# Performance work log

Measured on AMD Instinct MI355X. Metric: run time of the kernel, lower is better.

## Reference

```python
import jax, jax.numpy as jnp
import numpy as np

B = 2
C = 256
NH = 8
DH = C // NH
NL = 4
NP = 4
NLAYERS = 6
DFF = 1024
SHAPES = [(128, 128), (64, 64), (32, 32), (16, 16)]
LQ = sum(h * w for h, w in SHAPES)
STARTS = np.cumsum([0] + [h * w for h, w in SHAPES])[:-1].tolist()


def _ln(x, g, b, eps=1e-5):
    mu = jnp.mean(x, -1, keepdims=True)
    var = jnp.mean((x - mu) ** 2, -1, keepdims=True)
    return (x - mu) * jax.lax.rsqrt(var + eps) * g + b


def _ref_points():
    # centers of each cell, normalized to [0,1]; valid_ratios == 1 (masks=None path)
    pts = []
    for (h, w) in SHAPES:
        ry = (np.arange(h) + 0.5) / h
        rx = (np.arange(w) + 0.5) / w
        gy, gx = np.meshgrid(ry, rx, indexing='ij')
        pts.append(np.stack([gx.reshape(-1), gy.reshape(-1)], -1))
    return jnp.asarray(np.concatenate(pts, 0), jnp.float32)  # [LQ,2] (x,y)


def _bilinear(vf, loc, Hl, Wl):
    # vf: [B,NH,S,DH] flattened level features; loc: [B,LQ,NH,NP,2] in [0,1]
    # grid_sample semantics: bilinear, zero padding, align_corners=False
    x = loc[..., 0] * Wl - 0.5
    y = loc[..., 1] * Hl - 0.5
    x0 = jnp.floor(x)
    y0 = jnp.floor(y)
    wx = x - x0
    wy = y - y0
    out = 0.0
    for dx, dy, w in ((0, 0, (1 - wx) * (1 - wy)), (1, 0, wx * (1 - wy)),
                      (0, 1, (1 - wx) * wy), (1, 1, wx * wy)):
        xi = x0 + dx
        yi = y0 + dy
        valid = (xi >= 0) & (xi < Wl) & (yi >= 0) & (yi < Hl)
        idx = (jnp.clip(yi, 0, Hl - 1) * Wl + jnp.clip(xi, 0, Wl - 1)).astype(jnp.int32)
        idx = jnp.transpose(idx, (0, 2, 1, 3)).reshape(B, NH, -1)  # [B,NH,LQ*NP]
        g = jnp.take_along_axis(vf, idx[..., None], axis=2)        # [B,NH,LQ*NP,DH]
        wgt = jnp.transpose(w * valid, (0, 2, 1, 3)).reshape(B, NH, -1)
        out = out + g * wgt[..., None]
    return out.reshape(B, NH, LQ, NP, DH)


def _forward(src0, src1, src2, src3, pos0, pos1, pos2, pos3, level_embed,
             Woff, boff, Wattn, battn, Wval, bval, Wout, bout,
             g1, b1, Wff1, bff1, Wff2, bff2, g2, b2):
    srcs = [src0, src1, src2, src3]
    poss = [pos0, pos1, pos2, pos3]
    src = jnp.concatenate([s.reshape(B, C, -1).transpose(0, 2, 1) for s in srcs], 1)
    pos = jnp.concatenate([p.reshape(B, C, -1).transpose(0, 2, 1) + level_embed[l][None, None]
                           for l, p in enumerate(poss)], 1)
    ref = _ref_points()  # [LQ,2]
    norm_wh = jnp.asarray([[w, h] for (h, w) in SHAPES], jnp.float32)  # offset_normalizer
    x = src
    for l in range(NLAYERS):
        q = x + pos
        off = (q @ Woff[l] + boff[l]).reshape(B, LQ, NH, NL, NP, 2)
        attn = jax.nn.softmax((q @ Wattn[l] + battn[l]).reshape(B, LQ, NH, NL * NP), -1)
        attn = attn.reshape(B, LQ, NH, NL, NP)
        val = (x @ Wval[l] + bval[l]).reshape(B, LQ, NH, DH)
        loc = ref[None, :, None, None, None, :] + off / norm_wh[None, None, None, :, None, :]
        out = jnp.zeros((B, NH, LQ, DH), x.dtype)
        for lv, (h, w) in enumerate(SHAPES):
            s0 = STARTS[lv]
            vf = val[:, s0:s0 + h * w].transpose(0, 2, 1, 3)   # [B,NH,S,DH]
            samp = _bilinear(vf, loc[:, :, :, lv], h, w)       # [B,NH,LQ,NP,DH]
            a = attn[:, :, :, lv].transpose(0, 2, 1, 3)        # [B,NH,LQ,NP]
            out = out + jnp.einsum('bhqpd,bhqp->bhqd', samp, a)
        out = out.transpose(0, 2, 1, 3).reshape(B, LQ, C) @ Wout[l] + bout[l]
        x = _ln(x + out, g1[l], b1[l])
        ff = jax.nn.relu(x @ Wff1[l] + bff1[l]) @ Wff2[l] + bff2[l]
        x = _ln(x + ff, g2[l], b2[l])
    return x


def setup_inputs() -> dict:
    key = jax.random.key(0)
    ks = jax.random.split(key, 20)
    d = {}
    for i, (h, w) in enumerate(SHAPES):
        d[f'src{i}'] = jax.random.normal(ks[i], (B, C, h, w), jnp.float32)
        d[f'pos{i}'] = jax.random.normal(ks[4 + i], (B, C, h, w), jnp.float32) * 0.1
    d['level_embed'] = jax.random.normal(ks[8], (NL, C), jnp.float32)

    def lin(k, fi, fo, scale=None):
        s = scale if scale is not None else 1.0 / np.sqrt(fi)
        return jax.random.normal(k, (NLAYERS, fi, fo), jnp.float32) * s

    d['Woff'] = lin(ks[9], C, NH * NL * NP * 2, 0.01)
    d['boff'] = jax.random.uniform(ks[10], (NLAYERS, NH * NL * NP * 2), jnp.float32, -0.5, 0.5)
    d['Wattn'] = lin(ks[11], C, NH * NL * NP)
    d['battn'] = jnp.zeros((NLAYERS, NH * NL * NP), jnp.float32)
    d['Wval'] = lin(ks[12], C, C)
    d['bval'] = jnp.zeros((NLAYERS, C), jnp.float32)
    d['Wout'] = lin(ks[13], C, C)
    d['bout'] = jnp.zeros((NLAYERS, C), jnp.float32)
    d['g1'] = jnp.ones((NLAYERS, C), jnp.float32)
    d['b1'] = jnp.zeros((NLAYERS, C), jnp.float32)
    d['Wff1'] = lin(ks[14], C, DFF)
    d['bff1'] = jnp.zeros((NLAYERS, DFF), jnp.float32)
    d['Wff2'] = lin(ks[15], DFF, C)
    d['bff2'] = jnp.zeros((NLAYERS, C), jnp.float32)
    d['g2'] = jnp.ones((NLAYERS, C), jnp.float32)
    d['b2'] = jnp.zeros((NLAYERS, C), jnp.float32)
    return d


def reference(src0, src1, src2, src3, pos0, pos1, pos2, pos3, level_embed,
              Woff, boff, Wattn, battn, Wval, bval, Wout, bout,
              g1, b1, Wff1, bff1, Wff2, bff2, g2, b2):
    return _forward(src0, src1, src2, src3, pos0, pos1, pos2, pos3, level_embed,
                    Woff, boff, Wattn, battn, Wval, bval, Wout, bout,
                    g1, b1, Wff1, bff1, Wff2, bff2, g2, b2)
```

## Files before the change

kernel.cpp:

```cpp
#include <hip/hip_runtime.h>
#include <hip/hip_bf16.h>
#include <math.h>

namespace {
constexpr int B_   = 2;
constexpr int C_   = 256;
constexpr int NH_  = 8;
constexpr int DH_  = 32;
constexpr int NP_  = 4;
constexpr int DFF_ = 1024;
constexpr int LQ_  = 21760;
constexpr int M_   = B_ * LQ_;
}

typedef __bf16  bf16x8 __attribute__((ext_vector_type(8)));
typedef short   s16x8  __attribute__((ext_vector_type(8)));
typedef float   f32x4  __attribute__((ext_vector_type(4)));

static __device__ __forceinline__ unsigned short f2bf(float f) {
    return __builtin_bit_cast(unsigned short, __float2bfloat16(f));
}
static __device__ __forceinline__ float bf2f(unsigned short u) {
    return __bfloat162float(__builtin_bit_cast(__hip_bfloat16, u));
}

__global__ void k_wt(const float* __restrict__ in, __hip_bfloat16* __restrict__ out,
                     int K, int N, int outStride)
{
    __shared__ float tile[32][33];
    int n0 = blockIdx.x * 32, k0 = blockIdx.y * 32;
    const float* inl = in + (size_t)blockIdx.z * K * N;
    __hip_bfloat16* outl = out + (size_t)blockIdx.z * outStride;
    for (int i = threadIdx.y; i < 32; i += 8)
        tile[i][threadIdx.x] = inl[(size_t)(k0 + i) * N + n0 + threadIdx.x];
    __syncthreads();
    for (int i = threadIdx.y; i < 32; i += 8)
        outl[(size_t)(n0 + i) * K + k0 + threadIdx.x] = __float2bfloat16(tile[threadIdx.x][i]);
}

__global__ __launch_bounds__(256) void k_assemble2(
    const float* __restrict__ s0, const float* __restrict__ s1,
    const float* __restrict__ s2, const float* __restrict__ s3,
    const float* __restrict__ p0, const float* __restrict__ p1,
    const float* __restrict__ p2, const float* __restrict__ p3,
    const float* __restrict__ lev, float* __restrict__ x,
    __hip_bfloat16* __restrict__ xbf, __hip_bfloat16* __restrict__ posbf,
    __hip_bfloat16* __restrict__ qbf)
{
    int bid = blockIdx.x;
    int lv, rem, HW, S0;
    const float *sp, *pp;
    if (bid < 8192)       { lv = 0; rem = bid;         HW = 16384; S0 = 0;     sp = s0; pp = p0; }
    else if (bid < 10240) { lv = 1; rem = bid - 8192;  HW = 4096;  S0 = 16384; sp = s1; pp = p1; }
    else if (bid < 10752) { lv = 2; rem = bid - 10240; HW = 1024;  S0 = 20480; sp = s2; pp = p2; }
    else                  { lv = 3; rem = bid - 10752; HW = 256;   S0 = 21504; sp = s3; pp = p3; }
    int sptiles = HW >> 5;
    int spt = rem % sptiles;
    int ct  = (rem / sptiles) & 7;
    int b   = rem / (sptiles * 8);
    int sp0 = spt * 32, c0 = ct * 32;

    __shared__ float ts[32][33], tp[32][33];
    int tx = threadIdx.x & 31, ty = threadIdx.x >> 5;
#pragma unroll
    for (int i = 0; i < 4; i++) {
        int c = c0 + ty + i * 8;
        size_t si = ((size_t)(b * C_ + c)) * HW + sp0 + tx;
        ts[ty + i * 8][tx] = sp[si];
        tp[ty + i * 8][tx] = pp[si];
    }
    __syncthreads();
#pragma unroll
    for (int i = 0; i < 4; i++) {
        int s = S0 + sp0 + ty + i * 8;
        int c = c0 + tx;
        float sv = ts[tx][ty + i * 8];
        float pv = tp[tx][ty + i * 8] + lev[lv * C_ + c];
        size_t idx = ((size_t)(b * LQ_ + s)) * C_ + c;
        x[idx]     = sv;
        xbf[idx]   = __float2bfloat16(sv);
        posbf[idx] = __float2bfloat16(pv);
        qbf[idx]   = __float2bfloat16(sv + pv);
    }
}

template<bool RELU, bool BF16OUT>
__global__ __launch_bounds__(256) void k_gemm_mfma(
    const __hip_bfloat16* __restrict__ A,
    const __hip_bfloat16* __restrict__ Wt,
    const float* __restrict__ bias,
    void* __restrict__ Co,
    int M, int N, int K)
{
    __shared__ char As[128 * 128];
    __shared__ char Bs[128 * 128];
    int t = threadIdx.x, w = t >> 6, lane = t & 63;
    int m0 = blockIdx.x * 128, n0 = blockIdx.y * 128;
    int wm = w >> 1, wn = w & 1;

    f32x4 acc[4][4] = {};

    int rowoff  = lane >> 3;
    int colswz  = ((lane & 7) ^ (lane >> 3)) << 3;

    for (int kt = 0; kt < K; kt += 64) {
#pragma unroll
        for (int j = 0; j < 4; j++) {
            int rowbase = w * 32 + j * 8;
            const __hip_bfloat16* srcA = A  + (size_t)(m0 + rowbase + rowoff) * K + kt + colswz;
            const __hip_bfloat16* srcB = Wt + (size_t)(n0 + rowbase + rowoff) * K + kt + colswz;
            __builtin_amdgcn_global_load_lds(
                (const __attribute__((address_space(1))) void*)srcA,
                (__attribute__((address_space(3))) void*)(As + rowbase * 128), 16, 0, 0);
            __builtin_amdgcn_global_load_lds(
                (const __attribute__((address_space(1))) void*)srcB,
                (__attribute__((address_space(3))) void*)(Bs + rowbase * 128), 16, 0, 0);
        }
        __syncthreads();
#pragma unroll
        for (int k0 = 0; k0 < 64; k0 += 32) {
            int kb = k0 * 2 + (lane >> 4) * 16;
            bf16x8 af[4], bfr[4];
#pragma unroll
            for (int mi = 0; mi < 4; mi++) {
                int r = wm * 64 + mi * 16 + (lane & 15);
                s16x8 raw = *(const s16x8*)(As + r * 128 + (kb ^ ((r & 7) << 4)));
                af[mi] = __builtin_bit_cast(bf16x8, raw);
            }
#pragma unroll
            for (int ni = 0; ni < 4; ni++) {
                int r = wn * 64 + ni * 16 + (lane & 15);
                s16x8 raw = *(const s16x8*)(Bs + r * 128 + (kb ^ ((r & 7) << 4)));
                bfr[ni] = __builtin_bit_cast(bf16x8, raw);
            }
#pragma unroll
            for (int mi = 0; mi < 4; mi++)
#pragma unroll
                for (int ni = 0; ni < 4; ni++)
                    acc[mi][ni] = __builtin_amdgcn_mfma_f32_16x16x32_bf16(
                        af[mi], bfr[ni], acc[mi][ni], 0, 0, 0);
        }
        __syncthreads();
    }

#pragma unroll
    for (int ni = 0; ni < 4; ni++) {
        int col = n0 + wn * 64 + ni * 16 + (lane & 15);
        float bb = bias[col];
#pragma unroll
        for (int mi = 0; mi < 4; mi++) {
            int row = m0 + wm * 64 + mi * 16 + ((lane >> 4) << 2);
#pragma unroll
            for (int r = 0; r < 4; r++) {
                float v = acc[mi][ni][r] + bb;
                if (RELU) v = fmaxf(v, 0.f);
                if (BF16OUT)
                    ((__hip_bfloat16*)Co)[(size_t)(row + r) * N + col] = __float2bfloat16(v);
                else
                    ((float*)Co)[(size_t)(row + r) * N + col] = v;
            }
        }
    }
}

__global__ __launch_bounds__(256) void k_gemm_qa(
    const __hip_bfloat16* __restrict__ A,
    const __hip_bfloat16* __restrict__ Wq,
    const float* __restrict__ boff, const float* __restrict__ battn,
    float* __restrict__ offb, float* __restrict__ attb, int M)
{
    constexpr int K = 256;
    __shared__ char As[128 * 128];
    __shared__ char Bs[128 * 128];
    int t = threadIdx.x, w = t >> 6, lane = t & 63;
    int m0 = blockIdx.x * 128, n0 = blockIdx.y * 128;
    int wm = w >> 1, wn = w & 1;

    f32x4 acc[4][4] = {};
    int rowoff  = lane >> 3;
    int colswz  = ((lane & 7) ^ (lane >> 3)) << 3;

    for (int kt = 0; kt < K; kt += 64) {
#pragma unroll
        for (int j = 0; j < 4; j++) {
            int rowbase = w * 32 + j * 8;
            const __hip_bfloat16* srcA = A  + (size_t)(m0 + rowbase + rowoff) * K + kt + colswz;
            const __hip_bfloat16* srcB = Wq + (size_t)(n0 + rowbase + rowoff) * K + kt + colswz;
            __builtin_amdgcn_global_load_lds(
                (const __attribute__((address_space(1))) void*)srcA,
                (__attribute__((address_space(3))) void*)(As + rowbase * 128), 16, 0, 0);
            __builtin_amdgcn_global_load_lds(
                (const __attribute__((address_space(1))) void*)srcB,
                (__attribute__((address_space(3))) void*)(Bs + rowbase * 128), 16, 0, 0);
        }
        __syncthreads();
#pragma unroll
        for (int k0 = 0; k0 < 64; k0 += 32) {
            int kb = k0 * 2 + (lane >> 4) * 16;
            bf16x8 af[4], bfr[4];
#pragma unroll
            for (int mi = 0; mi < 4; mi++) {
                int r = wm * 64 + mi * 16 + (lane & 15);
                s16x8 raw = *(const s16x8*)(As + r * 128 + (kb ^ ((r & 7) << 4)));
                af[mi] = __builtin_bit_cast(bf16x8, raw);
            }
#pragma unroll
            for (int ni = 0; ni < 4; ni++) {
                int r = wn * 64 + ni * 16 + (lane & 15);
                s16x8 raw = *(const s16x8*)(Bs + r * 128 + (kb ^ ((r & 7) << 4)));
                bfr[ni] = __builtin_bit_cast(bf16x8, raw);
            }
#pragma unroll
            for (int mi = 0; mi < 4; mi++)
#pragma unroll
                for (int ni = 0; ni < 4; ni++)
                    acc[mi][ni] = __builtin_amdgcn_mfma_f32_16x16x32_bf16(
                        af[mi], bfr[ni], acc[mi][ni], 0, 0, 0);
        }
        __syncthreads();
    }

    bool isAttn = (blockIdx.y == 2);
    float* Co = isAttn ? attb : offb;
    int Nst   = isAttn ? 128 : 256;
    int cbase = isAttn ? 0 : n0;
    const float* bp = isAttn ? battn : boff;

#pragma unroll
    for (int ni = 0; ni < 4; ni++) {
        int col = cbase + wn * 64 + ni * 16 + (lane & 15);
        float bb = bp[col];
#pragma unroll
        for (int mi = 0; mi < 4; mi++) {
            int row = m0 + wm * 64 + mi * 16 + ((lane >> 4) << 2);
#pragma unroll
            for (int r = 0; r < 4; r++)
                Co[(size_t)(row + r) * Nst + col] = acc[mi][ni][r] + bb;
        }
    }
}

template<bool WRITE_Q>
__global__ __launch_bounds__(512) void k_gemm_ln(
    const __hip_bfloat16* __restrict__ A,
    const __hip_bfloat16* __restrict__ Wt,
    const float* __restrict__ bias,
    float* __restrict__ xio,
    __hip_bfloat16* __restrict__ xbf,
    const float* __restrict__ g, const float* __restrict__ beta,
    const __hip_bfloat16* __restrict__ posb,
    __hip_bfloat16* __restrict__ qout,
    int M, int K)
{
    __shared__ char As[128 * 128];
    __shared__ char Bs[256 * 128];
    __shared__ float sred1[128][4];
    __shared__ float sred2[128][4];

    int t = threadIdx.x, w = t >> 6, lane = t & 63;
    int m0 = blockIdx.x * 128;
    int wm = w >> 2, wn = w & 3;

    f32x4 acc[4][4] = {};

    int rowoff  = lane >> 3;
    int colswz  = ((lane & 7) ^ rowoff) << 3;

    for (int kt = 0; kt < K; kt += 64) {
#pragma unroll
        for (int j = 0; j < 2; j++) {
            int rowbase = w * 16 + j * 8;
            const __hip_bfloat16* srcA = A + (size_t)(m0 + rowbase + rowoff) * K + kt + colswz;
            __builtin_amdgcn_global_load_lds(
                (const __attribute__((address_space(1))) void*)srcA,
                (__attribute__((address_space(3))) void*)(As + rowbase * 128), 16, 0, 0);
        }
#pragma unroll
        for (int j = 0; j < 4; j++) {
            int rowbase = w * 32 + j * 8;
            const __hip_bfloat16* srcB = Wt + (size_t)(rowbase + rowoff) * K + kt + colswz;
            __builtin_amdgcn_global_load_lds(
                (const __attribute__((address_space(1))) void*)srcB,
                (__attribute__((address_space(3))) void*)(Bs + rowbase * 128), 16, 0, 0);
        }
        __syncthreads();
#pragma unroll
        for (int k0 = 0; k0 < 64; k0 += 32) {
            int kb = k0 * 2 + (lane >> 4) * 16;
            bf16x8 af[4], bfr[4];
#pragma unroll
            for (int mi = 0; mi < 4; mi++) {
                int r = wm * 64 + mi * 16 + (lane & 15);
                s16x8 raw = *(const s16x8*)(As + r * 128 + (kb ^ ((r & 7) << 4)));
                af[mi] = __builtin_bit_cast(bf16x8, raw);
            }
#pragma unroll
            for (int ni = 0; ni < 4; ni++) {
                int r = wn * 64 + ni * 16 + (lane & 15);
                s16x8 raw = *(const s16x8*)(Bs + r * 128 + (kb ^ ((r & 7) << 4)));
                bfr[ni] = __builtin_bit_cast(bf16x8, raw);
            }
#pragma unroll
            for (int mi = 0; mi < 4; mi++)
#pragma unroll
                for (int ni = 0; ni < 4; ni++)
                    acc[mi][ni] = __builtin_amdgcn_mfma_f32_16x16x32_bf16(
                        af[mi], bfr[ni], acc[mi][ni], 0, 0, 0);
        }
        __syncthreads();
    }

    int cl = lane & 15;
    int rg = (lane >> 4) << 2;
    float bcol[4], gcol[4], btcol[4];
#pragma unroll
    for (int ni = 0; ni < 4; ni++) {
        int col = wn * 64 + ni * 16 + cl;
        bcol[ni]  = bias[col];
        gcol[ni]  = g[col];
        btcol[ni] = beta[col];
    }

#pragma unroll
    for (int mi = 0; mi < 4; mi++)
#pragma unroll
    for (int r = 0; r < 4; r++) {
        int lr  = wm * 64 + mi * 16 + rg + r;
        int row = m0 + lr;
        float s = 0.f;
#pragma unroll
        for (int ni = 0; ni < 4; ni++) {
            int col = wn * 64 + ni * 16 + cl;
            float v = acc[mi][ni][r] + bcol[ni] + xio[(size_t)row * 256 + col];
            acc[mi][ni][r] = v;
            s += v;
        }
        s += __shfl_xor(s, 1); s += __shfl_xor(s, 2);
        s += __shfl_xor(s, 4); s += __shfl_xor(s, 8);
        if (cl == 0) sred1[lr][wn] = s;
    }
    __syncthreads();

    float mu[4][4];
#pragma unroll
    for (int mi = 0; mi < 4; mi++)
#pragma unroll
    for (int r = 0; r < 4; r++) {
        int lr = wm * 64 + mi * 16 + rg + r;
        mu[mi][r] = (sred1[lr][0] + sred1[lr][1] + sred1[lr][2] + sred1[lr][3]) * (1.f / 256.f);
        float s2 = 0.f;
#pragma unroll
        for (int ni = 0; ni < 4; ni++) {
            float d = acc[mi][ni][r] - mu[mi][r];
            s2 += d * d;
        }
        s2 += __shfl_xor(s2, 1); s2 += __shfl_xor(s2, 2);
        s2 += __shfl_xor(s2, 4); s2 += __shfl_xor(s2, 8);
        if (cl == 0) sred2[lr][wn] = s2;
    }
    __syncthreads();

#pragma unroll
    for (int mi = 0; mi < 4; mi++)
#pragma unroll
    for (int r = 0; r < 4; r++) {
        int lr  = wm * 64 + mi * 16 + rg + r;
        int row = m0 + lr;
        float var = (sred2[lr][0] + sred2[lr][1] + sred2[lr][2] + sred2[lr][3]) * (1.f / 256.f);
        float rstd = rsqrtf(var + 1e-5f);
#pragma unroll
        for (int ni = 0; ni < 4; ni++) {
            int col = wn * 64 + ni * 16 + cl;
            size_t idx = (size_t)row * 256 + col;
            float o = (acc[mi][ni][r] - mu[mi][r]) * rstd * gcol[ni] + btcol[ni];
            xio[idx] = o;
            xbf[idx] = __float2bfloat16(o);
            if (WRITE_Q)
                qout[idx] = __float2bfloat16(o + bf2f(__builtin_bit_cast(unsigned short, posb[idx])));
        }
    }
}

__global__ __launch_bounds__(256) void k_sample3(const __hip_bfloat16* __restrict__ val,
                                                 const float* __restrict__ off,
                                                 const float* __restrict__ logits,
                                                 __hip_bfloat16* __restrict__ out)
{
    __shared__ int2 sIW[4 * 32 * 16];

    int t  = threadIdx.x;
    int qb = blockIdx.x;

#pragma unroll
    for (int it = 0; it < 2; it++) {
        int item = t + it * 256;
        int qi = item >> 7;
        int pt = item & 127;
        int bs = qb * 4 + qi;
        int b  = bs / LQ_;
        int s  = bs % LQ_;
        int h  = pt >> 4, lv = (pt >> 2) & 3;

        float lg = logits[(size_t)bs * 128 + pt];
        float mx = lg;
#pragma unroll
        for (int m = 1; m < 16; m <<= 1) mx = fmaxf(mx, __shfl_xor(mx, m));
        float ex = __expf(lg - mx);
        float sm = ex;
#pragma unroll
        for (int m = 1; m < 16; m <<= 1) sm += __shfl_xor(sm, m);
        float aw = ex / sm;

        int p0, Wq;
        if (s < 16384)      { p0 = s;         Wq = 128; }
        else if (s < 20480) { p0 = s - 16384; Wq = 64;  }
        else if (s < 21504) { p0 = s - 20480; Wq = 32;  }
        else                { p0 = s - 21504; Wq = 16;  }
        float invWq = 1.f / (float)Wq;
        float refx = ((p0 % Wq) + 0.5f) * invWq;
        float refy = ((p0 / Wq) + 0.5f) * invWq;

        int W  = 128 >> lv;
        int S0 = (65536 - (65536 >> (2 * lv))) / 3;
        float fW = (float)W;

        float2 o2 = ((const float2*)(off + (size_t)bs * 256))[pt];
        float xx = refx * fW + o2.x - 0.5f;
        float yy = refy * fW + o2.y - 0.5f;
        float x0f = floorf(xx), y0f = floorf(yy);
        float wx = xx - x0f, wy = yy - y0f;
        int x0 = (int)x0f, y0 = (int)y0f;
        int x1 = x0 + 1, y1 = y0 + 1;
        bool vx0 = (x0 >= 0) & (x0 < W), vx1 = (x1 >= 0) & (x1 < W);
        bool vy0 = (y0 >= 0) & (y0 < W), vy1 = (y1 >= 0) & (y1 < W);
        int cx0 = min(max(x0, 0), W - 1), cx1 = min(max(x1, 0), W - 1);
        int cy0 = min(max(y0, 0), W - 1), cy1 = min(max(y1, 0), W - 1);

        int rowbase = (b * LQ_ + S0) * C_ + h * DH_;
        int g  = item >> 4;
        int pj = pt & 15;
        int i00 = (rowbase + (cy0 * W + cx0) * C_) * 2;
        int i10 = (rowbase + (cy0 * W + cx1) * C_) * 2;
        int i01 = (rowbase + (cy1 * W + cx0) * C_) * 2;
        int i11 = (rowbase + (cy1 * W + cx1) * C_) * 2;
        float w00 = aw * (1.f - wx) * (1.f - wy) * ((vx0 & vy0) ? 1.f : 0.f);
        float w10 = aw * wx * (1.f - wy) * ((vx1 & vy0) ? 1.f : 0.f);
        float w01 = aw * (1.f - wx) * wy * ((vx0 & vy1) ? 1.f : 0.f);
        float w11 = aw * wx * wy * ((vx1 & vy1) ? 1.f : 0.f);
        sIW[(0 * 32 + g) * 16 + pj] = make_int2(i00, __float_as_int(w00));
        sIW[(1 * 32 + g) * 16 + pj] = make_int2(i10, __float_as_int(w10));
        sIW[(2 * 32 + g) * 16 + pj] = make_int2(i01, __float_as_int(w01));
        sIW[(3 * 32 + g) * 16 + pj] = make_int2(i11, __float_as_int(w11));
    }
    __syncthreads();

    {
        int g  = t >> 3;
        int dq = t & 7;
        int bs = qb * 4 + (g >> 3);
        int h  = g & 7;
        int dbyte = dq * 8;

        const char* vbase = (const char*)val;
        float a0 = 0.f, a1 = 0.f, a2 = 0.f, a3 = 0.f;
#pragma unroll
        for (int j = 0; j < 16; j++) {
#pragma unroll
            for (int k = 0; k < 4; k++) {
                int2 iw = sIW[(k * 32 + g) * 16 + j];
                float w = __int_as_float(iw.y);
                uint2 u = *(const uint2*)(vbase + iw.x + dbyte);
                a0 = fmaf(w, __builtin_bit_cast(float, u.x << 16), a0);
                a1 = fmaf(w, __builtin_bit_cast(float, u.x & 0xffff0000u), a1);
                a2 = fmaf(w, __builtin_bit_cast(float, u.y << 16), a2);
                a3 = fmaf(w, __builtin_bit_cast(float, u.y & 0xffff0000u), a3);
            }
        }
        uint2 o;
        o.x = (unsigned)f2bf(a0) | ((unsigned)f2bf(a1) << 16);
        o.y = (unsigned)f2bf(a2) | ((unsigned)f2bf(a3) << 16);
        *(uint2*)((char*)out + (size_t)bs * 512 + h * 64 + dbyte) = o;
    }
}

extern "C" void kernel_launch(void* const* d_in, const int* in_sizes, int n_in,
                              void* d_out, int out_size, void* d_ws, size_t ws_size,
                              hipStream_t stream)
{
    const float* src_[4] = {(const float*)d_in[0], (const float*)d_in[2],
                            (const float*)d_in[4], (const float*)d_in[6]};
    const float* pos_[4] = {(const float*)d_in[1], (const float*)d_in[3],
                            (const float*)d_in[5], (const float*)d_in[7]};
    const float* lev   = (const float*)d_in[8];
    const float* Woff  = (const float*)d_in[9];
    const float* boff  = (const float*)d_in[10];
    const float* Wattn = (const float*)d_in[11];
    const float* battn = (const float*)d_in[12];
    const float* Wval  = (const float*)d_in[13];
    const float* bval  = (const float*)d_in[14];
    const float* Wout  = (const float*)d_in[15];
    const float* bout  = (const float*)d_in[16];
    const float* g1    = (const float*)d_in[17];
    const float* b1    = (const float*)d_in[18];
    const float* Wff1  = (const float*)d_in[19];
    const float* bff1  = (const float*)d_in[20];
    const float* Wff2  = (const float*)d_in[21];
    const float* bff2  = (const float*)d_in[22];
    const float* g2    = (const float*)d_in[23];
    const float* b2    = (const float*)d_in[24];

    float* x = (float*)d_out;
    size_t MC = (size_t)M_ * C_;

    __hip_bfloat16* pos_bf = (__hip_bfloat16*)d_ws;
    __hip_bfloat16* q_bf   = pos_bf + MC;
    __hip_bfloat16* x_bf   = q_bf + MC;
    float* offb = (float*)(x_bf + MC);
    float* attb = offb + MC;
    __hip_bfloat16* val_bf = (__hip_bfloat16*)(attb + (size_t)M_ * 128);
    __hip_bfloat16* ffh_bf = (__hip_bfloat16*)offb;
    __hip_bfloat16* wbf    = val_bf + MC;

    __hip_bfloat16* wq    = wbf;
    __hip_bfloat16* wvalt = wq    + 6 * 98304;
    __hip_bfloat16* woutt = wvalt + 6 * 65536;
    __hip_bfloat16* wff1t = woutt + 6 * 65536;
    __hip_bfloat16* wff2t = wff1t + 6 * 262144;

    dim3 blk(256);
    dim3 tblk(32, 8);

    k_wt<<<dim3(8, 8, 6),  tblk, 0, stream>>>(Woff,  wq,               256, 256,  98304);
    k_wt<<<dim3(4, 8, 6),  tblk, 0, stream>>>(Wattn, wq + 256 * 256,   256, 128,  98304);
    k_wt<<<dim3(8, 8, 6),  tblk, 0, stream>>>(Wval,  wvalt,            256, 256,  65536);
    k_wt<<<dim3(8, 8, 6),  tblk, 0, stream>>>(Wout,  woutt,            256, 256,  65536);
    k_wt<<<dim3(32, 8, 6), tblk, 0, stream>>>(Wff1,  wff1t,            256, 1024, 262144);
    k_wt<<<dim3(8, 32, 6), tblk, 0, stream>>>(Wff2,  wff2t,            1024, 256, 262144);

    k_assemble2<<<10880, blk, 0, stream>>>(
        src_[0], src_[1], src_[2], src_[3],
        pos_[0], pos_[1], pos_[2], pos_[3], lev, x, x_bf, pos_bf, q_bf);

    for (int l = 0; l < 6; l++) {
        k_gemm_qa<<<dim3(M_ / 128, 3), blk, 0, stream>>>(
            q_bf, wq + (size_t)l * 98304, boff + l * 256, battn + l * 128,
            offb, attb, M_);

        k_gemm_mfma<false, true><<<dim3(M_ / 128, 2), blk, 0, stream>>>(
            x_bf, wvalt + (size_t)l * 65536, bval + l * 256, val_bf, M_, 256, C_);

        k_sample3<<<M_ / 4, blk, 0, stream>>>(val_bf, offb, attb, q_bf);

        k_gemm_ln<false><<<M_ / 128, 512, 0, stream>>>(
            q_bf, woutt + (size_t)l * 65536, bout + l * 256,
            x, x_bf, g1 + l * 256, b1 + l * 256,
            nullptr, nullptr, M_, C_);

        k_gemm_mfma<true, true><<<dim3(M_ / 128, 8), blk, 0, stream>>>(
            x_bf, wff1t + (size_t)l * 262144, bff1 + l * DFF_, ffh_bf, M_, DFF_, C_);

        if (l < 5)
            k_gemm_ln<true><<<M_ / 128, 512, 0, stream>>>(
                ffh_bf, wff2t + (size_t)l * 262144, bff2 + l * C_,
                x, x_bf, g2 + l * 256, b2 + l * 256,
                pos_bf, q_bf, M_, DFF_);
        else
            k_gemm_ln<false><<<M_ / 128, 512, 0, stream>>>(
                ffh_bf, wff2t + (size_t)l * 262144, bff2 + l * C_,
                x, x_bf, g2 + l * 256, b2 + l * 256,
                nullptr, nullptr, M_, DFF_);
    }
}
```

Baseline: 1.971 ms.

## Store sampling offsets in fp16 and shrink LayerNorm GEMM tiles to 64 rows

The query-projection GEMM now writes the sampling offsets as fp16 instead of fp32, halving the offset buffer that the deformable sampling kernel reads. The fused GEMM+LayerNorm kernel changes from 128-row tiles with 8 warps to 64-row tiles with 4 warps, each warp covering a full 64-column slice. That doubles the grid size and reduces shared memory per block, which should improve occupancy and load balance. The tradeoff is fp16 rounding of offsets, which can shift sample locations slightly, and half the A-tile reuse of the weight tile per block.

New measurement: 2.042 ms. 3.6% more time.

```diff
diff --git a/kernel.cpp b/kernel.cpp
--- a/kernel.cpp
+++ b/kernel.cpp
@@ -1,5 +1,6 @@
 #include <hip/hip_runtime.h>
 #include <hip/hip_bf16.h>
+#include <hip/hip_fp16.h>
 #include <math.h>
 
 namespace {
@@ -167,7 +168,7 @@
     const __hip_bfloat16* __restrict__ A,
     const __hip_bfloat16* __restrict__ Wq,
     const float* __restrict__ boff, const float* __restrict__ battn,
-    float* __restrict__ offb, float* __restrict__ attb, int M)
+    __half* __restrict__ offh, float* __restrict__ attb, int M)
 {
     constexpr int K = 256;
     __shared__ char As[128 * 128];
@@ -220,28 +221,37 @@
         __syncthreads();
     }
 
-    bool isAttn = (blockIdx.y == 2);
-    float* Co = isAttn ? attb : offb;
-    int Nst   = isAttn ? 128 : 256;
-    int cbase = isAttn ? 0 : n0;
-    const float* bp = isAttn ? battn : boff;
-
-#pragma unroll
-    for (int ni = 0; ni < 4; ni++) {
-        int col = cbase + wn * 64 + ni * 16 + (lane & 15);
-        float bb = bp[col];
-#pragma unroll
-        for (int mi = 0; mi < 4; mi++) {
-            int row = m0 + wm * 64 + mi * 16 + ((lane >> 4) << 2);
-#pragma unroll
-            for (int r = 0; r < 4; r++)
-                Co[(size_t)(row + r) * Nst + col] = acc[mi][ni][r] + bb;
+    if (blockIdx.y == 2) {
+#pragma unroll
+        for (int ni = 0; ni < 4; ni++) {
+            int col = wn * 64 + ni * 16 + (lane & 15);
+            float bb = battn[col];
+#pragma unroll
+            for (int mi = 0; mi < 4; mi++) {
+                int row = m0 + wm * 64 + mi * 16 + ((lane >> 4) << 2);
+#pragma unroll
+                for (int r = 0; r < 4; r++)
+                    attb[(size_t)(row + r) * 128 + col] = acc[mi][ni][r] + bb;
+            }
+        }
+    } else {
+#pragma unroll
+        for (int ni = 0; ni < 4; ni++) {
+            int col = n0 + wn * 64 + ni * 16 + (lane & 15);
+            float bb = boff[col];
+#pragma unroll
+            for (int mi = 0; mi < 4; mi++) {
+                int row = m0 + wm * 64 + mi * 16 + ((lane >> 4) << 2);
+#pragma unroll
+                for (int r = 0; r < 4; r++)
+                    offh[(size_t)(row + r) * 256 + col] = __float2half(acc[mi][ni][r] + bb);
+            }
         }
     }
 }
 
 template<bool WRITE_Q>
-__global__ __launch_bounds__(512) void k_gemm_ln(
+__global__ __launch_bounds__(256) void k_gemm_ln(
     const __hip_bfloat16* __restrict__ A,
     const __hip_bfloat16* __restrict__ Wt,
     const float* __restrict__ bias,
@@ -252,14 +262,13 @@
     __hip_bfloat16* __restrict__ qout,
     int M, int K)
 {
-    __shared__ char As[128 * 128];
+    __shared__ char As[64 * 128];
     __shared__ char Bs[256 * 128];
-    __shared__ float sred1[128][4];
-    __shared__ float sred2[128][4];
+    __shared__ float sred1[64][4];
+    __shared__ float sred2[64][4];
 
     int t = threadIdx.x, w = t >> 6, lane = t & 63;
-    int m0 = blockIdx.x * 128;
-    int wm = w >> 2, wn = w & 3;
+    int m0 = blockIdx.x * 64;
 
     f32x4 acc[4][4] = {};
 
@@ -269,15 +278,15 @@
     for (int kt = 0; kt < K; kt += 64) {
 #pragma unroll
         for (int j = 0; j < 2; j++) {
-            int rowbase = w * 16 + j * 8;
+            int rowbase = w * 8 + j * 32;
             const __hip_bfloat16* srcA = A + (size_t)(m0 + rowbase + rowoff) * K + kt + colswz;
             __builtin_amdgcn_global_load_lds(
                 (const __attribute__((address_space(1))) void*)srcA,
                 (__attribute__((address_space(3))) void*)(As + rowbase * 128), 16, 0, 0);
         }
 #pragma unroll
-        for (int j = 0; j < 4; j++) {
-            int rowbase = w * 32 + j * 8;
+        for (int j = 0; j < 8; j++) {
+            int rowbase = w * 8 + j * 32;
             const __hip_bfloat16* srcB = Wt + (size_t)(rowbase + rowoff) * K + kt + colswz;
             __builtin_amdgcn_global_load_lds(
                 (const __attribute__((address_space(1))) void*)srcB,
@@ -290,13 +299,13 @@
             bf16x8 af[4], bfr[4];
 #pragma unroll
             for (int mi = 0; mi < 4; mi++) {
-                int r = wm * 64 + mi * 16 + (lane & 15);
+                int r = mi * 16 + (lane & 15);
                 s16x8 raw = *(const s16x8*)(As + r * 128 + (kb ^ ((r & 7) << 4)));
                 af[mi] = __builtin_bit_cast(bf16x8, raw);
             }
 #pragma unroll
             for (int ni = 0; ni < 4; ni++) {
-                int r = wn * 64 + ni * 16 + (lane & 15);
+                int r = w * 64 + ni * 16 + (lane & 15);
                 s16x8 raw = *(const s16x8*)(Bs + r * 128 + (kb ^ ((r & 7) << 4)));
                 bfr[ni] = __builtin_bit_cast(bf16x8, raw);
             }
@@ -315,7 +324,7 @@
     float bcol[4], gcol[4], btcol[4];
 #pragma unroll
     for (int ni = 0; ni < 4; ni++) {
-        int col = wn * 64 + ni * 16 + cl;
+        int col = w * 64 + ni * 16 + cl;
         bcol[ni]  = bias[col];
         gcol[ni]  = g[col];
         btcol[ni] = beta[col];
@@ -325,19 +334,19 @@
     for (int mi = 0; mi < 4; mi++)
 #pragma unroll
     for (int r = 0; r < 4; r++) {
-        int lr  = wm * 64 + mi * 16 + rg + r;
+        int lr  = mi * 16 + rg + r;
         int row = m0 + lr;
         float s = 0.f;
 #pragma unroll
         for (int ni = 0; ni < 4; ni++) {
-            int col = wn * 64 + ni * 16 + cl;
+            int col = w * 64 + ni * 16 + cl;
             float v = acc[mi][ni][r] + bcol[ni] + xio[(size_t)row * 256 + col];
             acc[mi][ni][r] = v;
             s += v;
         }
         s += __shfl_xor(s, 1); s += __shfl_xor(s, 2);
         s += __shfl_xor(s, 4); s += __shfl_xor(s, 8);
-        if (cl == 0) sred1[lr][wn] = s;
+        if (cl == 0) sred1[lr][w] = s;
     }
     __syncthreads();
 
@@ -346,7 +355,7 @@
     for (int mi = 0; mi < 4; mi++)
 #pragma unroll
     for (int r = 0; r < 4; r++) {
-        int lr = wm * 64 + mi * 16 + rg + r;
+        int lr = mi * 16 + rg + r;
         mu[mi][r] = (sred1[lr][0] + sred1[lr][1] + sred1[lr][2] + sred1[lr][3]) * (1.f / 256.f);
         float s2 = 0.f;
 #pragma unroll
@@ -356,7 +365,7 @@
         }
         s2 += __shfl_xor(s2, 1); s2 += __shfl_xor(s2, 2);
         s2 += __shfl_xor(s2, 4); s2 += __shfl_xor(s2, 8);
-        if (cl == 0) sred2[lr][wn] = s2;
+        if (cl == 0) sred2[lr][w] = s2;
     }
     __syncthreads();
 
@@ -364,13 +373,13 @@
     for (int mi = 0; mi < 4; mi++)
 #pragma unroll
     for (int r = 0; r < 4; r++) {
-        int lr  = wm * 64 + mi * 16 + rg + r;
+        int lr  = mi * 16 + rg + r;
         int row = m0 + lr;
         float var = (sred2[lr][0] + sred2[lr][1] + sred2[lr][2] + sred2[lr][3]) * (1.f / 256.f);
         float rstd = rsqrtf(var + 1e-5f);
 #pragma unroll
         for (int ni = 0; ni < 4; ni++) {
-            int col = wn * 64 + ni * 16 + cl;
+            int col = w * 64 + ni * 16 + cl;
             size_t idx = (size_t)row * 256 + col;
             float o = (acc[mi][ni][r] - mu[mi][r]) * rstd * gcol[ni] + btcol[ni];
             xio[idx] = o;
@@ -382,7 +391,7 @@
 }
 
 __global__ __launch_bounds__(256) void k_sample3(const __hip_bfloat16* __restrict__ val,
-                                                 const float* __restrict__ off,
+                                                 const __half* __restrict__ offh,
                                                  const float* __restrict__ logits,
                                                  __hip_bfloat16* __restrict__ out)
 {
@@ -424,9 +433,10 @@
         int S0 = (65536 - (65536 >> (2 * lv))) / 3;
         float fW = (float)W;
 
-        float2 o2 = ((const float2*)(off + (size_t)bs * 256))[pt];
-        float xx = refx * fW + o2.x - 0.5f;
-        float yy = refy * fW + o2.y - 0.5f;
+        __half2 o2 = ((const __half2*)(offh + (size_t)bs * 256))[pt];
+        float ox = __low2float(o2), oy = __high2float(o2);
+        float xx = refx * fW + ox - 0.5f;
+        float yy = refy * fW + oy - 0.5f;
         float x0f = floorf(xx), y0f = floorf(yy);
         float wx = xx - x0f, wy = yy - y0f;
         int x0 = (int)x0f, y0 = (int)y0f;
@@ -515,11 +525,12 @@
     __hip_bfloat16* pos_bf = (__hip_bfloat16*)d_ws;
     __hip_bfloat16* q_bf   = pos_bf + MC;
     __hip_bfloat16* x_bf   = q_bf + MC;
-    float* offb = (float*)(x_bf + MC);
-    float* attb = offb + MC;
+    __half* offh           = (__half*)(x_bf + MC);
+    float*  attb           = (float*)(offh + MC);
     __hip_bfloat16* val_bf = (__hip_bfloat16*)(attb + (size_t)M_ * 128);
-    __hip_bfloat16* ffh_bf = (__hip_bfloat16*)offb;
-    __hip_bfloat16* wbf    = val_bf + MC;
+    __hip_bfloat16* pad_bf = val_bf + MC;
+    __hip_bfloat16* ffh_bf = (__hip_bfloat16*)offh;
+    __hip_bfloat16* wbf    = pad_bf + MC;
 
     __hip_bfloat16* wq    = wbf;
     __hip_bfloat16* wvalt = wq    + 6 * 98304;
@@ -544,14 +555,14 @@
     for (int l = 0; l < 6; l++) {
         k_gemm_qa<<<dim3(M_ / 128, 3), blk, 0, stream>>>(
             q_bf, wq + (size_t)l * 98304, boff + l * 256, battn + l * 128,
-            offb, attb, M_);
+            offh, attb, M_);
 
         k_gemm_mfma<false, true><<<dim3(M_ / 128, 2), blk, 0, stream>>>(
             x_bf, wvalt + (size_t)l * 65536, bval + l * 256, val_bf, M_, 256, C_);
 
-        k_sample3<<<M_ / 4, blk, 0, stream>>>(val_bf, offb, attb, q_bf);
-
-        k_gemm_ln<false><<<M_ / 128, 512, 0, stream>>>(
+        k_sample3<<<M_ / 4, blk, 0, stream>>>(val_bf, offh, attb, q_bf);
+
+        k_gemm_ln<false><<<M_ / 64, blk, 0, stream>>>(
             q_bf, woutt + (size_t)l * 65536, bout + l * 256,
             x, x_bf, g1 + l * 256, b1 + l * 256,
             nullptr, nullptr, M_, C_);
@@ -560,12 +571,12 @@
             x_bf, wff1t + (size_t)l * 262144, bff1 + l * DFF_, ffh_bf, M_, DFF_, C_);
 
         if (l < 5)
-            k_gemm_ln<true><<<M_ / 128, 512, 0, stream>>>(
+            k_gemm_ln<true><<<M_ / 64, blk, 0, stream>>>(
                 ffh_bf, wff2t + (size_t)l * 262144, bff2 + l * C_,
                 x, x_bf, g2 + l * 256, b2 + l * 256,
                 pos_bf, q_bf, M_, DFF_);
         else
-            k_gemm_ln<false><<<M_ / 128, 512, 0, stream>>>(
+            k_gemm_ln<false><<<M_ / 64, blk, 0, stream>>>(
                 ffh_bf, wff2t + (size_t)l * 262144, bff2 + l * C_,
                 x, x_bf, g2 + l * 256, b2 + l * 256,
                 nullptr, nullptr, M_, DFF_);
```
